# Optimization experiments

Hardware: AMD Instinct MI355X
Metric: run time of the kernel (lower is better)

## Reference

```python
import jax, jax.numpy as jnp
import numpy as np

N_NODES = 100000
N_EDGES = 1600000


def _gcn_layer(h, edge_row, edge_col, edge_val, W):
    # GraphConvolution (eval mode, dropout skipped):
    # support = h @ W ; out = spmm(adj, support)
    support = h @ W                                   # [N, d_out]
    msg = support[edge_col] * edge_val[:, None]       # [E, d_out] gather
    return jax.ops.segment_sum(msg, edge_row, num_segments=N_NODES)


def setup_inputs() -> dict:
    key = jax.random.key(0)
    ks = jax.random.split(key, 7)
    x = jax.random.normal(ks[0], (N_NODES, 256), dtype=jnp.float32)
    edge_row = jax.random.randint(ks[1], (N_EDGES,), 0, N_NODES, dtype=jnp.int32)
    edge_col = jax.random.randint(ks[2], (N_EDGES,), 0, N_NODES, dtype=jnp.int32)
    edge_val = jax.random.uniform(ks[3], (N_EDGES,), dtype=jnp.float32)
    W1 = jax.random.normal(ks[4], (256, 128), dtype=jnp.float32) * 0.05
    W2 = jax.random.normal(ks[5], (128, 64), dtype=jnp.float32) * 0.05
    W3 = jax.random.normal(ks[6], (128, 64), dtype=jnp.float32) * 0.05
    return {"x": x, "edge_row": edge_row, "edge_col": edge_col,
            "edge_val": edge_val, "W1": W1, "W2": W2, "W3": W3}


def reference(x, edge_row, edge_col, edge_val, W1, W2, W3):
    hidden1 = jax.nn.relu(_gcn_layer(x, edge_row, edge_col, edge_val, W1))
    mu = _gcn_layer(hidden1, edge_row, edge_col, edge_val, W2)      # act = identity
    logvar = _gcn_layer(hidden1, edge_row, edge_col, edge_val, W3)  # act = identity
    # reparameterize: z_mu = mean(mu); z_logvar = log(mean(exp(logvar)))
    z_mu = jnp.mean(mu)
    z_logvar = jnp.log(jnp.mean(jnp.exp(logvar)))
    return (z_mu, z_logvar)
```

## Files before the change

kernel.cpp:

```cpp
#include <hip/hip_runtime.h>
#include <cstdint>
#include <cstddef>

namespace {

constexpr int NN = 100000;
constexpr int NE = 1600000;
constexpr int DI = 256;
constexpr int DH = 128;
constexpr int DO = 64;
constexpr int SCAN_CHUNK = 1024;
constexpr int SCAN_NB = (NN + SCAN_CHUNK - 1) / SCAN_CHUNK;
constexpr int RANK_NB = NE / 256;
constexpr int EDOT_NB = NE / 256;
constexpr int SP3_NB = NN / 32;
constexpr int G1_NB = (NN + 127) / 128;
constexpr int PREP_NB = (DI * DH + DH * DO) / 256;

using bf16x8 = __attribute__((ext_vector_type(8))) short;
using f32x4  = __attribute__((ext_vector_type(4))) float;

__device__ inline unsigned short f2bf(float f) {
  unsigned int u = __float_as_uint(f);
  u += 0x7FFFu + ((u >> 16) & 1u);
  return (unsigned short)(u >> 16);
}
__device__ inline float bflo(unsigned int u) { return __uint_as_float(u << 16); }
__device__ inline float bfhi(unsigned int u) { return __uint_as_float(u & 0xffff0000u); }

__device__ inline void fma8(float* acc, const uint4 g, const float v) {
  acc[0] = fmaf(v, bflo(g.x), acc[0]); acc[1] = fmaf(v, bfhi(g.x), acc[1]);
  acc[2] = fmaf(v, bflo(g.y), acc[2]); acc[3] = fmaf(v, bfhi(g.y), acc[3]);
  acc[4] = fmaf(v, bflo(g.z), acc[4]); acc[5] = fmaf(v, bfhi(g.z), acc[5]);
  acc[6] = fmaf(v, bflo(g.w), acc[6]); acc[7] = fmaf(v, bfhi(g.w), acc[7]);
}

__device__ __forceinline__ void gl16(const void* g, void* l) {
  __builtin_amdgcn_global_load_lds(
      (const __attribute__((address_space(1))) void*)g,
      (__attribute__((address_space(3))) void*)l, 16, 0, 0);
}

__device__ __forceinline__ bf16x8 pack8(const f32x4 lo, const f32x4 hi) {
  bf16x8 r;
  r[0] = (short)f2bf(lo[0]); r[1] = (short)f2bf(lo[1]);
  r[2] = (short)f2bf(lo[2]); r[3] = (short)f2bf(lo[3]);
  r[4] = (short)f2bf(hi[0]); r[5] = (short)f2bf(hi[1]);
  r[6] = (short)f2bf(hi[2]); r[7] = (short)f2bf(hi[3]);
  return r;
}

template <int BM, int BN, int BK, bool ABF16>
__device__ __forceinline__ void gemm_block(const void* __restrict__ Ap,
                                           const unsigned short* __restrict__ Bt,
                                           unsigned short* __restrict__ C,
                                           int M, int K, int bx) {
  constexpr int ABYT = ABF16 ? 2 : 4;
  constexpr int SBA = BK * ABYT;
  constexpr int SBB = BK * 2;
  constexpr int ASZ = BM * SBA;
  constexpr int BSZ = BN * SBB;
  constexpr int STAGE = ASZ + BSZ;
  constexpr int OUTP = BN + 8;
  constexpr int EP = (BM * OUTP * 2 > STAGE) ? 2 : 1;
  constexpr int ROWS_P = BM / EP;
  constexpr int OUTB = ROWS_P * OUTP * 2;
  constexpr int LDSB = STAGE > OUTB ? STAGE : OUTB;
  constexpr int AMSK = (SBA / 16 - 1) > 7 ? 7 : (SBA / 16 - 1);
  constexpr int BMSK = (SBB / 16 - 1) > 7 ? 7 : (SBB / 16 - 1);
  __shared__ __align__(16) char lds[LDSB];
  char* const as_ = lds;
  char* const bs_ = lds + ASZ;

  const int tid = threadIdx.x;
  const int wid = tid >> 6;
  const int lane = tid & 63;
  const int l15 = lane & 15;
  const int lg = lane >> 4;
  const int amsk = (l15 & AMSK) << 4;
  const int bmsk = (l15 & BMSK) << 4;
  const int row0 = bx * BM;

  constexpr int NGA = ASZ / (256 * 16);
  constexpr int NGB = BSZ / (256 * 16);
  const char* Ab = (const char*)Ap;
  const char* Bb = (const char*)Bt;

  f32x4 acc[2][BN / 16];
#pragma unroll
  for (int a = 0; a < 2; ++a)
#pragma unroll
    for (int b = 0; b < BN / 16; ++b) acc[a][b] = (f32x4)0.f;

  const int nk = K / BK;
  for (int t = 0; t < nk; ++t) {
    const int k0 = t * BK;
#pragma unroll
    for (int j = 0; j < NGA; ++j) {
      const int d = (j * 256 + tid) * 16;
      const int row = d / SBA;
      const int u = (d % SBA) ^ ((row & AMSK) << 4);
      int grow = row0 + row;
      if (grow >= M) grow = M - 1;
      gl16(Ab + (size_t)grow * (size_t)(K * ABYT) + k0 * ABYT + u, as_ + d);
    }
#pragma unroll
    for (int j = 0; j < NGB; ++j) {
      const int d = (j * 256 + tid) * 16;
      const int n = d / SBB;
      const int u = (d % SBB) ^ ((n & BMSK) << 4);
      gl16(Bb + (size_t)n * (size_t)(K * 2) + k0 * 2 + u, bs_ + d);
    }
    __syncthreads();
#pragma unroll
    for (int kk = 0; kk < BK; kk += 32) {
      const int koff = kk + lg * 8;
      bf16x8 a0, a1;
      if constexpr (!ABF16) {
        const int b0 = (wid * 32 + l15) * SBA + koff * 4;
        const int b1 = b0 + 16 * SBA;
        const f32x4 q00 = *(const f32x4*)(as_ + (b0 ^ amsk));
        const f32x4 q01 = *(const f32x4*)(as_ + ((b0 ^ amsk) ^ 16));
        const f32x4 q10 = *(const f32x4*)(as_ + (b1 ^ amsk));
        const f32x4 q11 = *(const f32x4*)(as_ + ((b1 ^ amsk) ^ 16));
        a0 = pack8(q00, q01);
        a1 = pack8(q10, q11);
      } else {
        const int b0 = (wid * 32 + l15) * SBA + koff * 2;
        const int b1 = b0 + 16 * SBA;
        a0 = *(const bf16x8*)(as_ + (b0 ^ amsk));
        a1 = *(const bf16x8*)(as_ + (b1 ^ amsk));
      }
#pragma unroll
      for (int nf = 0; nf < BN / 16; ++nf) {
        const int n = nf * 16 + l15;
        const bf16x8 b = *(const bf16x8*)(bs_ + ((n * SBB + koff * 2) ^ bmsk));
        acc[0][nf] = __builtin_amdgcn_mfma_f32_16x16x32_bf16(a0, b, acc[0][nf], 0, 0, 0);
        acc[1][nf] = __builtin_amdgcn_mfma_f32_16x16x32_bf16(a1, b, acc[1][nf], 0, 0, 0);
      }
    }
    __syncthreads();
  }
  unsigned short* outl = (unsigned short*)lds;
#pragma unroll
  for (int pp = 0; pp < EP; ++pp) {
    if ((wid * 32) / ROWS_P == pp || EP == 1) {
#pragma unroll
      for (int mf = 0; mf < 2; ++mf)
#pragma unroll
        for (int nf = 0; nf < BN / 16; ++nf)
#pragma unroll
          for (int r = 0; r < 4; ++r) {
            const int row = wid * 32 + mf * 16 + lg * 4 + r;
            const int col = nf * 16 + l15;
            outl[(row - pp * ROWS_P) * OUTP + col] = f2bf(acc[mf][nf][r]);
          }
    }
    __syncthreads();
#pragma unroll
    for (int i = tid; i < ROWS_P * (BN / 8); i += 256) {
      const int m = i / (BN / 8), c8 = i % (BN / 8);
      const int row = row0 + pp * ROWS_P + m;
      if (row < M)
        *(float4*)(&C[(size_t)row * BN + c8 * 8]) = *(const float4*)(&outl[m * OUTP + c8 * 8]);
    }
    if (EP > 1) __syncthreads();
  }
}

__global__ __launch_bounds__(256) void k_prep(const float* __restrict__ W1,
                                              const float* __restrict__ W3,
                                              unsigned short* __restrict__ w1t,
                                              unsigned short* __restrict__ w3t) {
  const int i = blockIdx.x * 256 + threadIdx.x;
  if (i < DI * DH) {
    const int n = i / DI, k = i % DI;
    w1t[i] = f2bf(W1[k * DH + n]);
  } else {
    const int j = i - DI * DH;
    const int n = j / DH, k = j % DH;
    w3t[j] = f2bf(W3[k * DO + n]);
  }
}

__global__ __launch_bounds__(256) void k_g1_rank(const float* __restrict__ x,
                                                 const unsigned short* __restrict__ w1t,
                                                 unsigned short* __restrict__ sup,
                                                 const int* __restrict__ erow,
                                                 int* __restrict__ cnt,
                                                 int* __restrict__ rank) {
  const int b = blockIdx.x;
  if (b % 9 == 0) {
    gemm_block<128, 128, 32, false>(x, w1t, sup, NN, DI, b / 9);
  } else {
    const int rb = (b / 9) * 8 + (b % 9) - 1;
    if (rb < RANK_NB) {
      const int e = rb * 256 + threadIdx.x;
      rank[e] = atomicAdd(&cnt[erow[e]], 1);
    }
  }
}

__global__ __launch_bounds__(256) void k_g2_edot(const unsigned short* __restrict__ h1,
                                                 const unsigned short* __restrict__ w3t,
                                                 unsigned short* __restrict__ sup,
                                                 const int* __restrict__ ecol,
                                                 const float* __restrict__ eval,
                                                 const float* __restrict__ hw,
                                                 float* __restrict__ pzmu) {
  const int b = blockIdx.x;
  if (b % 9 == 0) {
    gemm_block<128, 64, 64, true>(h1, w3t, sup, NN, DH, b / 9);
  } else {
    const int eb = (b / 9) * 8 + (b % 9) - 1;
    if (eb < EDOT_NB) {
      __shared__ float red[256];
      const int i = eb * 256 + threadIdx.x;
      red[threadIdx.x] = eval[i] * hw[ecol[i]];
      __syncthreads();
      for (int off = 128; off > 0; off >>= 1) {
        if (threadIdx.x < off) red[threadIdx.x] += red[threadIdx.x + off];
        __syncthreads();
      }
      if (threadIdx.x == 0) pzmu[eb] = red[0];
    }
  }
}

__global__ __launch_bounds__(256) void k_scan1(const int* __restrict__ cnt,
                                               int* __restrict__ bsum) {
  __shared__ int red[256];
  const int b = blockIdx.x, t = threadIdx.x;
  const int base = b * SCAN_CHUNK + t * 4;
  int s = 0;
#pragma unroll
  for (int j = 0; j < 4; ++j) {
    const int idx = base + j;
    if (idx < NN) s += cnt[idx];
  }
  red[t] = s;
  __syncthreads();
  for (int off = 128; off > 0; off >>= 1) {
    if (t < off) red[t] += red[t + off];
    __syncthreads();
  }
  if (t == 0) bsum[b] = red[0];
}

__global__ __launch_bounds__(128) void k_scan2(const int* __restrict__ bsum,
                                               int* __restrict__ boff,
                                               int* __restrict__ rowptr) {
  __shared__ int s[128];
  const int t = threadIdx.x;
  const int v = (t < SCAN_NB) ? bsum[t] : 0;
  s[t] = v;
  __syncthreads();
  for (int off = 1; off < 128; off <<= 1) {
    int x = 0;
    if (t >= off) x = s[t - off];
    __syncthreads();
    s[t] += x;
    __syncthreads();
  }
  if (t < SCAN_NB) boff[t] = s[t] - v;
  if (t == 127) rowptr[NN] = s[127];
}

__global__ __launch_bounds__(256) void k_scan3(const int* __restrict__ cnt,
                                               const int* __restrict__ boff,
                                               int* __restrict__ rowptr) {
  __shared__ int tsum[256];
  const int b = blockIdx.x, t = threadIdx.x;
  const int base = b * SCAN_CHUNK + t * 4;
  int v[4];
#pragma unroll
  for (int j = 0; j < 4; ++j) {
    const int idx = base + j;
    v[j] = (idx < NN) ? cnt[idx] : 0;
  }
  const int pre1 = v[0];
  const int pre2 = pre1 + v[1];
  const int pre3 = pre2 + v[2];
  const int s = pre3 + v[3];
  tsum[t] = s;
  __syncthreads();
  for (int off = 1; off < 256; off <<= 1) {
    int x = 0;
    if (t >= off) x = tsum[t - off];
    __syncthreads();
    tsum[t] += x;
    __syncthreads();
  }
  const int excl = tsum[t] - s + boff[b];
  const int w[4] = {excl, excl + pre1, excl + pre2, excl + pre3};
#pragma unroll
  for (int j = 0; j < 4; ++j) {
    const int idx = base + j;
    if (idx < NN) rowptr[idx] = w[j];
  }
}

__global__ __launch_bounds__(256) void k_place_w2(
    const int* __restrict__ erow, const int* __restrict__ ecol,
    const float* __restrict__ eval, const int* __restrict__ rank,
    const int* __restrict__ rowptr, int2* __restrict__ cpk,
    const float* __restrict__ W2, float* __restrict__ w2s) {
  const int b = blockIdx.x;
  if (b < RANK_NB) {
    const int e = b * 256 + threadIdx.x;
    const int pos = rowptr[erow[e]] + rank[e];
    cpk[pos] = make_int2(ecol[e], __float_as_int(eval[e]));
  } else {
    const int k = threadIdx.x;
    if (k < DH) {
      float s = 0.f;
      for (int d = 0; d < DO; ++d) s += W2[k * DO + d];
      w2s[k] = s;
    }
  }
}

__global__ __launch_bounds__(256) void k_spmm1(const unsigned short* __restrict__ sup1,
                                               const int* __restrict__ rowptr,
                                               const int2* __restrict__ cpk,
                                               const float* __restrict__ w2s,
                                               unsigned short* __restrict__ h1,
                                               float* __restrict__ hw) {
  const int tid = threadIdx.x;
  const int lane = tid & 15;
  const int r = blockIdx.x * 16 + (tid >> 4);
  const int e0 = rowptr[r];
  const int e1 = rowptr[r + 1];
  const uint4* s8 = reinterpret_cast<const uint4*>(sup1);
  float aA[8] = {0,0,0,0,0,0,0,0}, aB[8] = {0,0,0,0,0,0,0,0};
  float aC[8] = {0,0,0,0,0,0,0,0}, aD[8] = {0,0,0,0,0,0,0,0};
  int e = e0;
  for (; e + 4 <= e1; e += 4) {
    const int2 p0 = cpk[e],     p1 = cpk[e + 1];
    const int2 p2 = cpk[e + 2], p3 = cpk[e + 3];
    const uint4 g0 = s8[(size_t)p0.x * 16 + lane];
    const uint4 g1 = s8[(size_t)p1.x * 16 + lane];
    const uint4 g2 = s8[(size_t)p2.x * 16 + lane];
    const uint4 g3 = s8[(size_t)p3.x * 16 + lane];
    fma8(aA, g0, __int_as_float(p0.y));
    fma8(aB, g1, __int_as_float(p1.y));
    fma8(aC, g2, __int_as_float(p2.y));
    fma8(aD, g3, __int_as_float(p3.y));
  }
  if (e + 2 <= e1) {
    const int2 p0 = cpk[e], p1 = cpk[e + 1];
    const uint4 g0 = s8[(size_t)p0.x * 16 + lane];
    const uint4 g1 = s8[(size_t)p1.x * 16 + lane];
    fma8(aA, g0, __int_as_float(p0.y));
    fma8(aB, g1, __int_as_float(p1.y));
    e += 2;
  }
  if (e < e1) {
    const int2 p0 = cpk[e];
    const uint4 g0 = s8[(size_t)p0.x * 16 + lane];
    fma8(aC, g0, __int_as_float(p0.y));
  }
  float acc[8];
#pragma unroll
  for (int j = 0; j < 8; ++j) acc[j] = fmaxf((aA[j] + aB[j]) + (aC[j] + aD[j]), 0.f);
  uint4 o;
  o.x = (unsigned)f2bf(acc[0]) | ((unsigned)f2bf(acc[1]) << 16);
  o.y = (unsigned)f2bf(acc[2]) | ((unsigned)f2bf(acc[3]) << 16);
  o.z = (unsigned)f2bf(acc[4]) | ((unsigned)f2bf(acc[5]) << 16);
  o.w = (unsigned)f2bf(acc[6]) | ((unsigned)f2bf(acc[7]) << 16);
  reinterpret_cast<uint4*>(h1)[(size_t)r * 16 + lane] = o;
  const float4 wlo = reinterpret_cast<const float4*>(w2s)[lane * 2];
  const float4 whi = reinterpret_cast<const float4*>(w2s)[lane * 2 + 1];
  float p = acc[0] * wlo.x + acc[1] * wlo.y + acc[2] * wlo.z + acc[3] * wlo.w +
            acc[4] * whi.x + acc[5] * whi.y + acc[6] * whi.z + acc[7] * whi.w;
#pragma unroll
  for (int off = 8; off > 0; off >>= 1) p += __shfl_down(p, off, 16);
  if (lane == 0) hw[r] = p;
}

__global__ __launch_bounds__(256) void k_spmm3(const unsigned short* __restrict__ sup3,
                                               const int* __restrict__ rowptr,
                                               const int2* __restrict__ cpk,
                                               float* __restrict__ pexp) {
  const int tid = threadIdx.x;
  const int lane = tid & 7;
  const int r = blockIdx.x * 32 + (tid >> 3);
  const int e0 = rowptr[r];
  const int e1 = rowptr[r + 1];
  const uint4* s8 = reinterpret_cast<const uint4*>(sup3);
  float aA[8] = {0,0,0,0,0,0,0,0}, aB[8] = {0,0,0,0,0,0,0,0};
  float aC[8] = {0,0,0,0,0,0,0,0}, aD[8] = {0,0,0,0,0,0,0,0};
  int e = e0;
  for (; e + 4 <= e1; e += 4) {
    const int2 p0 = cpk[e],     p1 = cpk[e + 1];
    const int2 p2 = cpk[e + 2], p3 = cpk[e + 3];
    const uint4 g0 = s8[(size_t)p0.x * 8 + lane];
    const uint4 g1 = s8[(size_t)p1.x * 8 + lane];
    const uint4 g2 = s8[(size_t)p2.x * 8 + lane];
    const uint4 g3 = s8[(size_t)p3.x * 8 + lane];
    fma8(aA, g0, __int_as_float(p0.y));
    fma8(aB, g1, __int_as_float(p1.y));
    fma8(aC, g2, __int_as_float(p2.y));
    fma8(aD, g3, __int_as_float(p3.y));
  }
  if (e + 2 <= e1) {
    const int2 p0 = cpk[e], p1 = cpk[e + 1];
    const uint4 g0 = s8[(size_t)p0.x * 8 + lane];
    const uint4 g1 = s8[(size_t)p1.x * 8 + lane];
    fma8(aA, g0, __int_as_float(p0.y));
    fma8(aB, g1, __int_as_float(p1.y));
    e += 2;
  }
  if (e < e1) {
    const int2 p0 = cpk[e];
    const uint4 g0 = s8[(size_t)p0.x * 8 + lane];
    fma8(aC, g0, __int_as_float(p0.y));
  }
  float p = 0.f;
#pragma unroll
  for (int j = 0; j < 8; ++j) p += expf((aA[j] + aB[j]) + (aC[j] + aD[j]));
#pragma unroll
  for (int off = 4; off > 0; off >>= 1) p += __shfl_down(p, off, 8);
  __shared__ float part[32];
  if (lane == 0) part[tid >> 3] = p;
  __syncthreads();
  if (tid == 0) {
    float s = 0.f;
#pragma unroll
    for (int i = 0; i < 32; ++i) s += part[i];
    pexp[blockIdx.x] = s;
  }
}

__global__ __launch_bounds__(256) void k_final(const float* __restrict__ pzmu, int nz,
                                               const float* __restrict__ pexp, int ne,
                                               float* __restrict__ out) {
  __shared__ float red[256];
  const int t = threadIdx.x;
  float s1 = 0.f, s2 = 0.f;
  for (int i = t; i < nz; i += 256) s1 += pzmu[i];
  for (int i = t; i < ne; i += 256) s2 += pexp[i];
  red[t] = s1;
  __syncthreads();
  for (int off = 128; off > 0; off >>= 1) {
    if (t < off) red[t] += red[t + off];
    __syncthreads();
  }
  const float tot1 = red[0];
  __syncthreads();
  red[t] = s2;
  __syncthreads();
  for (int off = 128; off > 0; off >>= 1) {
    if (t < off) red[t] += red[t + off];
    __syncthreads();
  }
  if (t == 0) {
    const float denom = (float)NN * (float)DO;
    out[0] = tot1 / denom;
    out[1] = logf(red[0] / denom);
  }
}

}

extern "C" void kernel_launch(void* const* d_in, const int* in_sizes, int n_in,
                              void* d_out, int out_size, void* d_ws, size_t ws_size,
                              hipStream_t stream) {
  const float* x    = (const float*)d_in[0];
  const int*   erow = (const int*)d_in[1];
  const int*   ecol = (const int*)d_in[2];
  const float* eval = (const float*)d_in[3];
  const float* W1   = (const float*)d_in[4];
  const float* W2   = (const float*)d_in[5];
  const float* W3   = (const float*)d_in[6];
  float* out = (float*)d_out;

  char* p = (char*)d_ws;
  auto alloc = [&](size_t bytes) -> void* {
    void* r = (void*)p;
    p += (bytes + 255) & ~(size_t)255;
    return r;
  };
  unsigned short* sup = (unsigned short*)alloc((size_t)NN * DH * 2);
  unsigned short* h1  = (unsigned short*)alloc((size_t)NN * DH * 2);
  int2*  cpk    = (int2*)alloc((size_t)NE * 8);
  int*   rank   = (int*)alloc((size_t)NE * 4);
  int*   rowptr = (int*)alloc((size_t)(NN + 1) * 4);
  int*   cnt    = (int*)alloc((size_t)NN * 4);
  float* hw     = (float*)alloc((size_t)NN * 4);
  float* w2s    = (float*)alloc(DH * 4);
  unsigned short* w1t = (unsigned short*)alloc((size_t)DH * DI * 2);
  unsigned short* w3t = (unsigned short*)alloc((size_t)DO * DH * 2);
  int*   bsum   = (int*)alloc(SCAN_NB * 4);
  int*   boff   = (int*)alloc(SCAN_NB * 4);
  float* pexp   = (float*)alloc(SP3_NB * 4);
  float* pzmu   = (float*)alloc(EDOT_NB * 4);

  hipMemsetAsync(cnt, 0, (size_t)NN * 4, stream);

  k_prep<<<PREP_NB, 256, 0, stream>>>(W1, W3, w1t, w3t);

  k_g1_rank<<<G1_NB * 9, 256, 0, stream>>>(x, w1t, sup, erow, cnt, rank);

  k_scan1<<<SCAN_NB, 256, 0, stream>>>(cnt, bsum);
  k_scan2<<<1, 128, 0, stream>>>(bsum, boff, rowptr);
  k_scan3<<<SCAN_NB, 256, 0, stream>>>(cnt, boff, rowptr);

  k_place_w2<<<RANK_NB + 1, 256, 0, stream>>>(erow, ecol, eval, rank, rowptr, cpk, W2, w2s);

  k_spmm1<<<NN / 16, 256, 0, stream>>>(sup, rowptr, cpk, w2s, h1, hw);

  k_g2_edot<<<G1_NB * 9, 256, 0, stream>>>(h1, w3t, sup, ecol, eval, hw, pzmu);

  k_spmm3<<<NN / 32, 256, 0, stream>>>(sup, rowptr, cpk, pexp);

  k_final<<<1, 256, 0, stream>>>(pzmu, EDOT_NB, pexp, SP3_NB, out);
}
```

Baseline: 238.5 us.

## Replace global-atomic CSR build with two-level bucketed counting sort

New measurement: 200.3 us. 1.19x faster.

```diff
diff --git a/kernel.cpp b/kernel.cpp
--- a/kernel.cpp
+++ b/kernel.cpp
@@ -9,9 +9,9 @@
 constexpr int DI = 256;
 constexpr int DH = 128;
 constexpr int DO = 64;
-constexpr int SCAN_CHUNK = 1024;
-constexpr int SCAN_NB = (NN + SCAN_CHUNK - 1) / SCAN_CHUNK;
-constexpr int RANK_NB = NE / 256;
+constexpr int EPB = 1024;
+constexpr int NBA = (NE + EPB - 1) / EPB;
+constexpr int NBUK = (NN + 255) / 256;
 constexpr int EDOT_NB = NE / 256;
 constexpr int SP3_NB = NN / 32;
 constexpr int G1_NB = (NN + 127) / 128;
@@ -183,140 +183,148 @@
   }
 }
 
-__global__ __launch_bounds__(256) void k_g1_rank(const float* __restrict__ x,
-                                                 const unsigned short* __restrict__ w1t,
-                                                 unsigned short* __restrict__ sup,
-                                                 const int* __restrict__ erow,
-                                                 int* __restrict__ cnt,
-                                                 int* __restrict__ rank) {
+__global__ __launch_bounds__(256) void k_passA(const int* __restrict__ erow,
+                                               int* __restrict__ gcnt,
+                                               unsigned short* __restrict__ rank8) {
+  __shared__ int h[NBUK];
+  const int tid = threadIdx.x, k = blockIdx.x;
+  for (int i = tid; i < NBUK; i += 256) h[i] = 0;
+  __syncthreads();
+  const int e0 = k * EPB;
+#pragma unroll
+  for (int j = 0; j < 4; ++j) {
+    const int e = e0 + j * 256 + tid;
+    if (e < NE) rank8[e] = (unsigned short)atomicAdd(&h[erow[e] >> 8], 1);
+  }
+  __syncthreads();
+  for (int i = tid; i < NBUK; i += 256) gcnt[(size_t)k * NBUK + i] = h[i];
+}
+
+__global__ __launch_bounds__(256) void k_passB1(const int* __restrict__ gcnt,
+                                                int* __restrict__ boff,
+                                                int* __restrict__ btot) {
+  const int b = blockIdx.x, t = threadIdx.x;
+  int v[7];
+  int s = 0;
+#pragma unroll
+  for (int j = 0; j < 7; ++j) {
+    const int k = t * 7 + j;
+    v[j] = (k < NBA) ? gcnt[(size_t)k * NBUK + b] : 0;
+    s += v[j];
+  }
+  __shared__ int ps[256];
+  ps[t] = s;
+  __syncthreads();
+  for (int off = 1; off < 256; off <<= 1) {
+    int x = (t >= off) ? ps[t - off] : 0;
+    __syncthreads();
+    ps[t] += x;
+    __syncthreads();
+  }
+  int excl = ps[t] - s;
+  if (t == 255) btot[b] = ps[255];
+#pragma unroll
+  for (int j = 0; j < 7; ++j) {
+    const int k = t * 7 + j;
+    if (k < NBA) boff[(size_t)b * NBA + k] = excl;
+    excl += v[j];
+  }
+}
+
+__global__ __launch_bounds__(256) void k_passB2(const int* __restrict__ btot,
+                                                int* __restrict__ bbase,
+                                                int* __restrict__ rowptr,
+                                                const float* __restrict__ W2,
+                                                float* __restrict__ w2s) {
+  if (blockIdx.x == 1) {
+    const int kk = threadIdx.x;
+    if (kk < DH) {
+      float s = 0.f;
+      for (int d = 0; d < DO; ++d) s += W2[kk * DO + d];
+      w2s[kk] = s;
+    }
+    return;
+  }
+  __shared__ int sdat[512];
+  const int t = threadIdx.x;
+  sdat[t] = (t < NBUK) ? btot[t] : 0;
+  sdat[t + 256] = (t + 256 < NBUK) ? btot[t + 256] : 0;
+  __syncthreads();
+  for (int off = 1; off < 512; off <<= 1) {
+    const int x0 = (t >= off) ? sdat[t - off] : 0;
+    const int x1 = (t + 256 >= off) ? sdat[t + 256 - off] : 0;
+    __syncthreads();
+    sdat[t] += x0;
+    sdat[t + 256] += x1;
+    __syncthreads();
+  }
+  if (t == 0) { bbase[0] = 0; rowptr[NN] = NE; }
+  bbase[t + 1] = sdat[t];
+  if (t + 257 <= NBUK) bbase[t + 257] = sdat[t + 256];
+}
+
+__global__ __launch_bounds__(256) void k_cg1(const float* __restrict__ x,
+                                             const unsigned short* __restrict__ w1t,
+                                             unsigned short* __restrict__ sup,
+                                             const int* __restrict__ erow,
+                                             const int* __restrict__ ecol,
+                                             const float* __restrict__ eval,
+                                             const unsigned short* __restrict__ rank8,
+                                             const int* __restrict__ boff,
+                                             const int* __restrict__ bbase,
+                                             uint2* __restrict__ scv) {
   const int b = blockIdx.x;
-  if (b % 9 == 0) {
-    gemm_block<128, 128, 32, false>(x, w1t, sup, NN, DI, b / 9);
+  if (b < G1_NB) {
+    gemm_block<128, 128, 32, false>(x, w1t, sup, NN, DI, b);
   } else {
-    const int rb = (b / 9) * 8 + (b % 9) - 1;
-    if (rb < RANK_NB) {
-      const int e = rb * 256 + threadIdx.x;
-      rank[e] = atomicAdd(&cnt[erow[e]], 1);
-    }
-  }
-}
-
-__global__ __launch_bounds__(256) void k_g2_edot(const unsigned short* __restrict__ h1,
-                                                 const unsigned short* __restrict__ w3t,
-                                                 unsigned short* __restrict__ sup,
-                                                 const int* __restrict__ ecol,
-                                                 const float* __restrict__ eval,
-                                                 const float* __restrict__ hw,
-                                                 float* __restrict__ pzmu) {
-  const int b = blockIdx.x;
-  if (b % 9 == 0) {
-    gemm_block<128, 64, 64, true>(h1, w3t, sup, NN, DH, b / 9);
-  } else {
-    const int eb = (b / 9) * 8 + (b % 9) - 1;
-    if (eb < EDOT_NB) {
-      __shared__ float red[256];
-      const int i = eb * 256 + threadIdx.x;
-      red[threadIdx.x] = eval[i] * hw[ecol[i]];
-      __syncthreads();
-      for (int off = 128; off > 0; off >>= 1) {
-        if (threadIdx.x < off) red[threadIdx.x] += red[threadIdx.x + off];
-        __syncthreads();
+    const int k = b - G1_NB;
+    const int e0 = k * EPB;
+    const int tid = threadIdx.x;
+#pragma unroll
+    for (int j = 0; j < 4; ++j) {
+      const int e = e0 + j * 256 + tid;
+      if (e < NE) {
+        const int r = erow[e];
+        const int bu = r >> 8;
+        const int pos = bbase[bu] + boff[(size_t)bu * NBA + k] + (int)rank8[e];
+        scv[pos] = make_uint2(((unsigned)(r & 255) << 17) | (unsigned)ecol[e],
+                              __float_as_uint(eval[e]));
       }
-      if (threadIdx.x == 0) pzmu[eb] = red[0];
-    }
-  }
-}
-
-__global__ __launch_bounds__(256) void k_scan1(const int* __restrict__ cnt,
-                                               int* __restrict__ bsum) {
-  __shared__ int red[256];
+    }
+  }
+}
+
+__global__ __launch_bounds__(256) void k_passD(const uint2* __restrict__ scv,
+                                               const int* __restrict__ bbase,
+                                               int* __restrict__ rowptr,
+                                               int2* __restrict__ cpk) {
   const int b = blockIdx.x, t = threadIdx.x;
-  const int base = b * SCAN_CHUNK + t * 4;
-  int s = 0;
-#pragma unroll
-  for (int j = 0; j < 4; ++j) {
-    const int idx = base + j;
-    if (idx < NN) s += cnt[idx];
-  }
-  red[t] = s;
-  __syncthreads();
-  for (int off = 128; off > 0; off >>= 1) {
-    if (t < off) red[t] += red[t + off];
-    __syncthreads();
-  }
-  if (t == 0) bsum[b] = red[0];
-}
-
-__global__ __launch_bounds__(128) void k_scan2(const int* __restrict__ bsum,
-                                               int* __restrict__ boff,
-                                               int* __restrict__ rowptr) {
-  __shared__ int s[128];
-  const int t = threadIdx.x;
-  const int v = (t < SCAN_NB) ? bsum[t] : 0;
-  s[t] = v;
-  __syncthreads();
-  for (int off = 1; off < 128; off <<= 1) {
-    int x = 0;
-    if (t >= off) x = s[t - off];
-    __syncthreads();
-    s[t] += x;
-    __syncthreads();
-  }
-  if (t < SCAN_NB) boff[t] = s[t] - v;
-  if (t == 127) rowptr[NN] = s[127];
-}
-
-__global__ __launch_bounds__(256) void k_scan3(const int* __restrict__ cnt,
-                                               const int* __restrict__ boff,
-                                               int* __restrict__ rowptr) {
-  __shared__ int tsum[256];
-  const int b = blockIdx.x, t = threadIdx.x;
-  const int base = b * SCAN_CHUNK + t * 4;
-  int v[4];
-#pragma unroll
-  for (int j = 0; j < 4; ++j) {
-    const int idx = base + j;
-    v[j] = (idx < NN) ? cnt[idx] : 0;
-  }
-  const int pre1 = v[0];
-  const int pre2 = pre1 + v[1];
-  const int pre3 = pre2 + v[2];
-  const int s = pre3 + v[3];
-  tsum[t] = s;
+  const int lo = bbase[b], hi = bbase[b + 1];
+  __shared__ int c1[256], sc[256];
+  c1[t] = 0;
+  __syncthreads();
+  for (int e = lo + t; e < hi; e += 256) atomicAdd(&c1[scv[e].x >> 17], 1);
+  __syncthreads();
+  const int my = c1[t];
+  sc[t] = my;
   __syncthreads();
   for (int off = 1; off < 256; off <<= 1) {
-    int x = 0;
-    if (t >= off) x = tsum[t - off];
-    __syncthreads();
-    tsum[t] += x;
-    __syncthreads();
-  }
-  const int excl = tsum[t] - s + boff[b];
-  const int w[4] = {excl, excl + pre1, excl + pre2, excl + pre3};
-#pragma unroll
-  for (int j = 0; j < 4; ++j) {
-    const int idx = base + j;
-    if (idx < NN) rowptr[idx] = w[j];
-  }
-}
-
-__global__ __launch_bounds__(256) void k_place_w2(
-    const int* __restrict__ erow, const int* __restrict__ ecol,
-    const float* __restrict__ eval, const int* __restrict__ rank,
-    const int* __restrict__ rowptr, int2* __restrict__ cpk,
-    const float* __restrict__ W2, float* __restrict__ w2s) {
-  const int b = blockIdx.x;
-  if (b < RANK_NB) {
-    const int e = b * 256 + threadIdx.x;
-    const int pos = rowptr[erow[e]] + rank[e];
-    cpk[pos] = make_int2(ecol[e], __float_as_int(eval[e]));
-  } else {
-    const int k = threadIdx.x;
-    if (k < DH) {
-      float s = 0.f;
-      for (int d = 0; d < DO; ++d) s += W2[k * DO + d];
-      w2s[k] = s;
-    }
+    const int xx = (t >= off) ? sc[t - off] : 0;
+    __syncthreads();
+    sc[t] += xx;
+    __syncthreads();
+  }
+  const int ro = sc[t] - my;
+  const int gr = b * 256 + t;
+  if (gr < NN) rowptr[gr] = lo + ro;
+  c1[t] = 0;
+  sc[t] = ro;
+  __syncthreads();
+  for (int e = lo + t; e < hi; e += 256) {
+    const uint2 q = scv[e];
+    const int i = (int)(q.x >> 17);
+    const int p = lo + sc[i] + atomicAdd(&c1[i], 1);
+    cpk[p] = make_int2((int)(q.x & 0x1FFFFu), (int)q.y);
   }
 }
 
@@ -378,6 +386,32 @@
   if (lane == 0) hw[r] = p;
 }
 
+__global__ __launch_bounds__(256) void k_g2_edot(const unsigned short* __restrict__ h1,
+                                                 const unsigned short* __restrict__ w3t,
+                                                 unsigned short* __restrict__ sup,
+                                                 const int* __restrict__ ecol,
+                                                 const float* __restrict__ eval,
+                                                 const float* __restrict__ hw,
+                                                 float* __restrict__ pzmu) {
+  const int b = blockIdx.x;
+  if (b % 9 == 0) {
+    gemm_block<128, 64, 64, true>(h1, w3t, sup, NN, DH, b / 9);
+  } else {
+    const int eb = (b / 9) * 8 + (b % 9) - 1;
+    if (eb < EDOT_NB) {
+      __shared__ float red[256];
+      const int i = eb * 256 + threadIdx.x;
+      red[threadIdx.x] = eval[i] * hw[ecol[i]];
+      __syncthreads();
+      for (int off = 128; off > 0; off >>= 1) {
+        if (threadIdx.x < off) red[threadIdx.x] += red[threadIdx.x + off];
+        __syncthreads();
+      }
+      if (threadIdx.x == 0) pzmu[eb] = red[0];
+    }
+  }
+}
+
 __global__ __launch_bounds__(256) void k_spmm3(const unsigned short* __restrict__ sup3,
                                                const int* __restrict__ rowptr,
                                                const int2* __restrict__ cpk,
@@ -484,29 +518,28 @@
   unsigned short* sup = (unsigned short*)alloc((size_t)NN * DH * 2);
   unsigned short* h1  = (unsigned short*)alloc((size_t)NN * DH * 2);
   int2*  cpk    = (int2*)alloc((size_t)NE * 8);
-  int*   rank   = (int*)alloc((size_t)NE * 4);
+  uint2* scv    = (uint2*)alloc((size_t)NE * 8);
+  unsigned short* rank8 = (unsigned short*)alloc((size_t)NE * 2);
   int*   rowptr = (int*)alloc((size_t)(NN + 1) * 4);
-  int*   cnt    = (int*)alloc((size_t)NN * 4);
+  int*   gcnt   = (int*)alloc((size_t)NBA * NBUK * 4);
+  int*   boff   = (int*)alloc((size_t)NBUK * NBA * 4);
+  int*   btot   = (int*)alloc((size_t)NBUK * 4);
+  int*   bbase  = (int*)alloc((size_t)(NBUK + 1) * 4);
   float* hw     = (float*)alloc((size_t)NN * 4);
   float* w2s    = (float*)alloc(DH * 4);
   unsigned short* w1t = (unsigned short*)alloc((size_t)DH * DI * 2);
   unsigned short* w3t = (unsigned short*)alloc((size_t)DO * DH * 2);
-  int*   bsum   = (int*)alloc(SCAN_NB * 4);
-  int*   boff   = (int*)alloc(SCAN_NB * 4);
   float* pexp   = (float*)alloc(SP3_NB * 4);
   float* pzmu   = (float*)alloc(EDOT_NB * 4);
 
-  hipMemsetAsync(cnt, 0, (size_t)NN * 4, stream);
-
   k_prep<<<PREP_NB, 256, 0, stream>>>(W1, W3, w1t, w3t);
 
-  k_g1_rank<<<G1_NB * 9, 256, 0, stream>>>(x, w1t, sup, erow, cnt, rank);
-
-  k_scan1<<<SCAN_NB, 256, 0, stream>>>(cnt, bsum);
-  k_scan2<<<1, 128, 0, stream>>>(bsum, boff, rowptr);
-  k_scan3<<<SCAN_NB, 256, 0, stream>>>(cnt, boff, rowptr);
-
-  k_place_w2<<<RANK_NB + 1, 256, 0, stream>>>(erow, ecol, eval, rank, rowptr, cpk, W2, w2s);
+  k_passA<<<NBA, 256, 0, stream>>>(erow, gcnt, rank8);
+  k_passB1<<<NBUK, 256, 0, stream>>>(gcnt, boff, btot);
+  k_passB2<<<2, 256, 0, stream>>>(btot, bbase, rowptr, W2, w2s);
+  k_cg1<<<G1_NB + NBA, 256, 0, stream>>>(x, w1t, sup, erow, ecol, eval,
+                                         rank8, boff, bbase, scv);
+  k_passD<<<NBUK, 256, 0, stream>>>(scv, bbase, rowptr, cpk);
 
   k_spmm1<<<NN / 16, 256, 0, stream>>>(sup, rowptr, cpk, w2s, h1, hw);
 
```
